# Performance work log

Measured on AMD Instinct MI355X. Metric: run time of the kernel, lower is better.

The kernel has to match this reference:

```python
import jax, jax.numpy as jnp
import numpy as np

C = 1.0
TEMPERATURE = 1.0
EPS = 1e-10
N, D = 8192, 512


def setup_inputs() -> dict:
    key = jax.random.key(0)
    k1, k2 = jax.random.split(key)
    # scale so embeddings lie inside the unit (Poincare) ball: norms ~0.5
    scale = 0.5 / np.sqrt(D)
    audio = jax.random.normal(k1, (N, D), dtype=jnp.float32) * scale
    text = jax.random.normal(k2, (N, D), dtype=jnp.float32) * scale
    labels = jnp.arange(N, dtype=jnp.int32)
    return {"audio_features": audio, "text_features": text, "labels": labels}


def _hyperbolic_similarity(a, b):
    # pairwise squared distance via norm expansion (avoids N x N x D tensor)
    a2 = jnp.sum(a * a, axis=-1)            # [N]
    b2 = jnp.sum(b * b, axis=-1)            # [M]
    diff_sq = a2[:, None] + b2[None, :] - 2.0 * (a @ b.T)  # [N, M]
    a2c = jnp.minimum(a2, 1.0 - EPS)
    b2c = jnp.minimum(b2, 1.0 - EPS)
    denom = jnp.maximum((1.0 - a2c)[:, None] * (1.0 - b2c)[None, :], EPS)
    arg = jnp.maximum(1.0 + 2.0 * diff_sq / denom, 1.0 + EPS)
    dist = jnp.arccosh(arg) / jnp.sqrt(jnp.asarray(C, a.dtype))
    return -dist / TEMPERATURE


def _cross_entropy(logits, labels):
    logp = jax.nn.log_softmax(logits, axis=-1)
    picked = jnp.take_along_axis(logp, labels[:, None], axis=-1)[:, 0]
    return -jnp.mean(picked)


def reference(audio_features, text_features, labels):
    sim = _hyperbolic_similarity(audio_features, text_features)  # [N, M]
    loss_audio = _cross_entropy(sim, labels)
    loss_text = _cross_entropy(sim.T, labels)
    return (loss_audio + loss_text) * 0.5
```

## Files before the change

kernel.cpp:

```cpp
#include <hip/hip_runtime.h>
#include <hip/hip_bf16.h>


#define NROWS 8192
#define DDIM  512
#define BM 128
#define BN 128
#define BK 64
#define NT (DDIM / BK)
#define LDSBUF 32768

typedef __attribute__((ext_vector_type(8))) short bf16x8;
typedef __attribute__((ext_vector_type(4))) float f32x4;

constexpr float EPSF = 1e-10f;

#define GLOAD_LDS16(g, l)                                                        \
    __builtin_amdgcn_global_load_lds(                                            \
        (const __attribute__((address_space(1))) void*)(g),                      \
        (__attribute__((address_space(3))) void*)(l), 16, 0, 0)

__device__ inline unsigned short f2bf(float f) {
    union { float f; unsigned int u; } x; x.f = f;
    unsigned int r = x.u + 0x7fffu + ((x.u >> 16) & 1u);
    return (unsigned short)(r >> 16);
}

__global__ __launch_bounds__(256) void convert_norms(const float* __restrict__ audio,
                                                     const float* __restrict__ text,
                                                     unsigned short* __restrict__ Ab,
                                                     unsigned short* __restrict__ Bb,
                                                     float* __restrict__ a2,
                                                     float* __restrict__ b2,
                                                     float* __restrict__ diag) {
    int wave = threadIdx.x >> 6;
    int lane = threadIdx.x & 63;
    int row  = blockIdx.x * 4 + wave;
    const float* ra = audio + (size_t)row * DDIM + lane * 8;
    const float* rt = text  + (size_t)row * DDIM + lane * 8;
    float4 a0 = *(const float4*)(ra), a1 = *(const float4*)(ra + 4);
    float4 t0 = *(const float4*)(rt), t1 = *(const float4*)(rt + 4);

    float sa = a0.x*a0.x + a0.y*a0.y + a0.z*a0.z + a0.w*a0.w
             + a1.x*a1.x + a1.y*a1.y + a1.z*a1.z + a1.w*a1.w;
    float st = t0.x*t0.x + t0.y*t0.y + t0.z*t0.z + t0.w*t0.w
             + t1.x*t1.x + t1.y*t1.y + t1.z*t1.z + t1.w*t1.w;
    float dt = a0.x*t0.x + a0.y*t0.y + a0.z*t0.z + a0.w*t0.w
             + a1.x*t1.x + a1.y*t1.y + a1.z*t1.z + a1.w*t1.w;

    unsigned short ua[8], ut[8];
    ua[0]=f2bf(a0.x); ua[1]=f2bf(a0.y); ua[2]=f2bf(a0.z); ua[3]=f2bf(a0.w);
    ua[4]=f2bf(a1.x); ua[5]=f2bf(a1.y); ua[6]=f2bf(a1.z); ua[7]=f2bf(a1.w);
    ut[0]=f2bf(t0.x); ut[1]=f2bf(t0.y); ut[2]=f2bf(t0.z); ut[3]=f2bf(t0.w);
    ut[4]=f2bf(t1.x); ut[5]=f2bf(t1.y); ut[6]=f2bf(t1.z); ut[7]=f2bf(t1.w);
    *(uint4*)(Ab + (size_t)row * DDIM + lane * 8) = *(const uint4*)ua;
    *(uint4*)(Bb + (size_t)row * DDIM + lane * 8) = *(const uint4*)ut;

    #pragma unroll
    for (int m = 1; m < 64; m <<= 1) {
        sa += __shfl_xor(sa, m);
        st += __shfl_xor(st, m);
        dt += __shfl_xor(dt, m);
    }
    if (lane == 0) {
        a2[row] = sa;
        b2[row] = st;
        float a2c  = fminf(sa, 1.0f - EPSF);
        float b2c  = fminf(st, 1.0f - EPSF);
        float diff = sa + st - 2.0f * dt;
        float den  = fmaxf((1.0f - a2c) * (1.0f - b2c), EPSF);
        float arg  = fmaxf(1.0f + 2.0f * diff / den, 1.0f + EPSF);
        diag[row]  = -logf(arg + sqrtf(arg * arg - 1.0f));
    }
}

__global__ __launch_bounds__(512, 4) void hyper_gemm(
    const unsigned short* __restrict__ A, const unsigned short* __restrict__ B,
    const float* __restrict__ a2, const float* __restrict__ b2,
    float* __restrict__ rowsum, float* __restrict__ colsum) {

    __shared__ char lds[2 * LDSBUF];

    const int tid  = threadIdx.x;
    const int lane = tid & 63;
    const int w    = tid >> 6;
    const int wm   = w >> 2;
    const int wn   = w & 3;

    const int bid = blockIdx.x;
    const int idx = bid >> 3;
    const int by  = (bid & 7) * 8 + (idx & 7);
    const int bx  = idx >> 3;
    const int i0 = by * BM;
    const int j0 = bx * BN;

    const int g  = lane >> 4;
    const int cl = lane & 15;

    const int srow = lane >> 3;
    const int scol = ((lane & 7) ^ srow) * 8;
    const char* aP[2]; const char* bP[2]; int ldsOff[2];
    #pragma unroll
    for (int c = 0; c < 2; ++c) {
        int row = w * 16 + c * 8 + srow;
        aP[c] = (const char*)(A + (size_t)(i0 + row) * DDIM + scol);
        bP[c] = (const char*)(B + (size_t)(j0 + row) * DDIM + scol);
        ldsOff[c] = w * 2048 + c * 1024;
    }

    int offA[4][2], offB[2][2];
    #pragma unroll
    for (int mi = 0; mi < 4; ++mi) {
        int rowA = wm * 64 + mi * 16 + cl;
        #pragma unroll
        for (int kh = 0; kh < 2; ++kh) {
            int cb = (kh * 32 + g * 8) * 2;
            offA[mi][kh] = rowA * 128 + (cb ^ ((rowA & 7) << 4));
        }
    }
    #pragma unroll
    for (int ni = 0; ni < 2; ++ni) {
        int rowB = wn * 32 + ni * 16 + cl;
        #pragma unroll
        for (int kh = 0; kh < 2; ++kh) {
            int cb = (kh * 32 + g * 8) * 2;
            offB[ni][kh] = 16384 + rowB * 128 + (cb ^ ((rowB & 7) << 4));
        }
    }

    f32x4 acc[4][2];
    #pragma unroll
    for (int mi = 0; mi < 4; ++mi)
        #pragma unroll
        for (int ni = 0; ni < 2; ++ni)
            acc[mi][ni] = (f32x4)0.0f;

#define STAGE(buf, t)                                                     \
    do {                                                                  \
        _Pragma("unroll")                                                 \
        for (int c = 0; c < 2; ++c) {                                     \
            GLOAD_LDS16(aP[c] + (t) * (BK * 2),                           \
                        lds + (buf) * LDSBUF + ldsOff[c]);                \
            GLOAD_LDS16(bP[c] + (t) * (BK * 2),                           \
                        lds + (buf) * LDSBUF + 16384 + ldsOff[c]);        \
        }                                                                 \
    } while (0)

#define COMPUTE(buf)                                                      \
    do {                                                                  \
        _Pragma("unroll")                                                 \
        for (int kh = 0; kh < 2; ++kh) {                                  \
            bf16x8 af[4], bv[2];                                          \
            _Pragma("unroll")                                             \
            for (int mi = 0; mi < 4; ++mi)                                \
                af[mi] = *(const bf16x8*)(lds + (buf) * LDSBUF + offA[mi][kh]); \
            _Pragma("unroll")                                             \
            for (int ni = 0; ni < 2; ++ni)                                \
                bv[ni] = *(const bf16x8*)(lds + (buf) * LDSBUF + offB[ni][kh]); \
            _Pragma("unroll")                                             \
            for (int mi = 0; mi < 4; ++mi)                                \
                _Pragma("unroll")                                         \
                for (int ni = 0; ni < 2; ++ni)                            \
                    acc[mi][ni] = __builtin_amdgcn_mfma_f32_16x16x32_bf16(\
                        af[mi], bv[ni], acc[mi][ni], 0, 0, 0);            \
        }                                                                 \
    } while (0)

    STAGE(0, 0);
    __syncthreads();
    #pragma unroll
    for (int t = 0; t < NT; ++t) {
        if (t + 1 < NT) STAGE((t + 1) & 1, t + 1);
        COMPUTE(t & 1);
        if (t + 1 < NT) __syncthreads();
    }
#undef STAGE
#undef COMPUTE

    float B2c[2], fb[2];
    #pragma unroll
    for (int ni = 0; ni < 2; ++ni) {
        float B2 = b2[j0 + wn * 32 + ni * 16 + cl];
        B2c[ni] = B2;
        fb[ni] = __builtin_amdgcn_rcpf(1.0f - fminf(B2, 1.0f - EPSF));
    }

    float cp[2] = {0.f, 0.f};
    #pragma unroll
    for (int mi = 0; mi < 4; ++mi) {
        #pragma unroll
        for (int reg = 0; reg < 4; ++reg) {
            int   gi  = i0 + wm * 64 + mi * 16 + g * 4 + reg;
            float A2  = a2[gi];
            float fa  = 2.0f * __builtin_amdgcn_rcpf(1.0f - fminf(A2, 1.0f - EPSF));
            float rsum = 0.f;
            #pragma unroll
            for (int ni = 0; ni < 2; ++ni) {
                float dot  = acc[mi][ni][reg];
                float diff = fmaf(-2.0f, dot, A2 + B2c[ni]);
                float arg  = fmaf(diff * fa, fb[ni], 1.0f);
                arg = fmaxf(arg, 1.0f);
                float sq = sqrtf(fmaf(arg, arg, -1.0f));
                float e  = arg - sq;
                rsum += e;
                cp[ni] += e;
            }
            float v = rsum;
            v += __shfl_xor(v, 1); v += __shfl_xor(v, 2);
            v += __shfl_xor(v, 4); v += __shfl_xor(v, 8);
            if (cl == 0) atomicAdd(&rowsum[gi], v);
        }
    }
    #pragma unroll
    for (int ni = 0; ni < 2; ++ni) {
        float v = cp[ni];
        v += __shfl_xor(v, 16); v += __shfl_xor(v, 32);
        if (g == 0) atomicAdd(&colsum[j0 + wn * 32 + ni * 16 + cl], v);
    }
}

__global__ __launch_bounds__(1024) void finalize(const float* __restrict__ rowsum,
                                                 const float* __restrict__ colsum,
                                                 const float* __restrict__ diag,
                                                 float* __restrict__ out) {
    float s = 0.f;
    for (int i = threadIdx.x; i < NROWS; i += 1024)
        s += logf(rowsum[i]) + logf(colsum[i]) - 2.0f * diag[i];
    __shared__ float red[16];
    int lane = threadIdx.x & 63, wv = threadIdx.x >> 6;
    #pragma unroll
    for (int m = 1; m < 64; m <<= 1) s += __shfl_xor(s, m);
    if (lane == 0) red[wv] = s;
    __syncthreads();
    if (threadIdx.x == 0) {
        float t = 0.f;
        #pragma unroll
        for (int k = 0; k < 16; ++k) t += red[k];
        out[0] = t / (2.0f * NROWS);
    }
}

extern "C" void kernel_launch(void* const* d_in, const int* in_sizes, int n_in,
                              void* d_out, int out_size, void* d_ws, size_t ws_size,
                              hipStream_t stream) {
    const float* audio = (const float*)d_in[0];
    const float* text  = (const float*)d_in[1];
    float* out = (float*)d_out;

    char* ws = (char*)d_ws;
    const size_t BF = (size_t)NROWS * DDIM * sizeof(unsigned short);
    unsigned short* Abf = (unsigned short*)ws;
    unsigned short* Bbf = (unsigned short*)(ws + BF);
    float* a2     = (float*)(ws + 2 * BF);
    float* b2     = a2 + NROWS;
    float* rowsum = b2 + NROWS;
    float* colsum = rowsum + NROWS;
    float* diag   = colsum + NROWS;

    hipMemsetAsync(rowsum, 0, 2 * NROWS * sizeof(float), stream);
    convert_norms<<<NROWS / 4, 256, 0, stream>>>(audio, text, Abf, Bbf, a2, b2, diag);
    hyper_gemm<<<(NROWS / BM) * (NROWS / BN), 512, 0, stream>>>(Abf, Bbf, a2, b2, rowsum, colsum);
    finalize<<<1, 1024, 0, stream>>>(rowsum, colsum, diag, out);
}
```

Measured before the change: 229.1 us.

## Switch GEMM operands from bf16 to scaled fp8 e4m3 MFMA and fold memset

New measurement: 212.6 us. 1.08x faster.

```diff
diff --git a/kernel.cpp b/kernel.cpp
--- a/kernel.cpp
+++ b/kernel.cpp
@@ -6,33 +6,48 @@
 #define DDIM  512
 #define BM 128
 #define BN 128
-#define BK 64
+#define BK 128
 #define NT (DDIM / BK)
 #define LDSBUF 32768
 
-typedef __attribute__((ext_vector_type(8))) short bf16x8;
 typedef __attribute__((ext_vector_type(4))) float f32x4;
 
 constexpr float EPSF = 1e-10f;
+constexpr float DOT_SCALE = 1.0f / 1024.0f;
 
 #define GLOAD_LDS16(g, l)                                                        \
     __builtin_amdgcn_global_load_lds(                                            \
         (const __attribute__((address_space(1))) void*)(g),                      \
         (__attribute__((address_space(3))) void*)(l), 16, 0, 0)
 
-__device__ inline unsigned short f2bf(float f) {
+__device__ inline unsigned int f2e4m3(float f) {
     union { float f; unsigned int u; } x; x.f = f;
-    unsigned int r = x.u + 0x7fffu + ((x.u >> 16) & 1u);
-    return (unsigned short)(r >> 16);
+    unsigned int s = (x.u >> 24) & 0x80u;
+    float af = __builtin_fabsf(f);
+    unsigned int r;
+    if (af >= 0.015625f) {
+        unsigned int m = x.u & 0x7fffffffu;
+        m += 0x000fffffu + ((m >> 20) & 1u);
+        r = ((m >> 20) - (120u << 3)) & 0x7fu;
+    } else {
+        int q = (int)rintf(af * 512.0f);
+        r = (unsigned int)q;
+    }
+    return r | s;
 }
 
 __global__ __launch_bounds__(256) void convert_norms(const float* __restrict__ audio,
                                                      const float* __restrict__ text,
-                                                     unsigned short* __restrict__ Ab,
-                                                     unsigned short* __restrict__ Bb,
+                                                     unsigned char* __restrict__ Aq,
+                                                     unsigned char* __restrict__ Bq,
                                                      float* __restrict__ a2,
                                                      float* __restrict__ b2,
-                                                     float* __restrict__ diag) {
+                                                     float* __restrict__ diag,
+                                                     float* __restrict__ zbuf) {
+    if (blockIdx.x < 32) {
+        int z = blockIdx.x * 512 + threadIdx.x * 2;
+        *(float2*)(zbuf + z) = make_float2(0.f, 0.f);
+    }
     int wave = threadIdx.x >> 6;
     int lane = threadIdx.x & 63;
     int row  = blockIdx.x * 4 + wave;
@@ -48,13 +63,17 @@
     float dt = a0.x*t0.x + a0.y*t0.y + a0.z*t0.z + a0.w*t0.w
              + a1.x*t1.x + a1.y*t1.y + a1.z*t1.z + a1.w*t1.w;
 
-    unsigned short ua[8], ut[8];
-    ua[0]=f2bf(a0.x); ua[1]=f2bf(a0.y); ua[2]=f2bf(a0.z); ua[3]=f2bf(a0.w);
-    ua[4]=f2bf(a1.x); ua[5]=f2bf(a1.y); ua[6]=f2bf(a1.z); ua[7]=f2bf(a1.w);
-    ut[0]=f2bf(t0.x); ut[1]=f2bf(t0.y); ut[2]=f2bf(t0.z); ut[3]=f2bf(t0.w);
-    ut[4]=f2bf(t1.x); ut[5]=f2bf(t1.y); ut[6]=f2bf(t1.z); ut[7]=f2bf(t1.w);
-    *(uint4*)(Ab + (size_t)row * DDIM + lane * 8) = *(const uint4*)ua;
-    *(uint4*)(Bb + (size_t)row * DDIM + lane * 8) = *(const uint4*)ut;
+    uint2 pa, pt;
+    pa.x = f2e4m3(a0.x*32.f) | (f2e4m3(a0.y*32.f) << 8) |
+           (f2e4m3(a0.z*32.f) << 16) | (f2e4m3(a0.w*32.f) << 24);
+    pa.y = f2e4m3(a1.x*32.f) | (f2e4m3(a1.y*32.f) << 8) |
+           (f2e4m3(a1.z*32.f) << 16) | (f2e4m3(a1.w*32.f) << 24);
+    pt.x = f2e4m3(t0.x*32.f) | (f2e4m3(t0.y*32.f) << 8) |
+           (f2e4m3(t0.z*32.f) << 16) | (f2e4m3(t0.w*32.f) << 24);
+    pt.y = f2e4m3(t1.x*32.f) | (f2e4m3(t1.y*32.f) << 8) |
+           (f2e4m3(t1.z*32.f) << 16) | (f2e4m3(t1.w*32.f) << 24);
+    *(uint2*)(Aq + (size_t)row * DDIM + lane * 8) = pa;
+    *(uint2*)(Bq + (size_t)row * DDIM + lane * 8) = pt;
 
     #pragma unroll
     for (int m = 1; m < 64; m <<= 1) {
@@ -75,7 +94,7 @@
 }
 
 __global__ __launch_bounds__(512, 4) void hyper_gemm(
-    const unsigned short* __restrict__ A, const unsigned short* __restrict__ B,
+    const unsigned char* __restrict__ A, const unsigned char* __restrict__ B,
     const float* __restrict__ a2, const float* __restrict__ b2,
     float* __restrict__ rowsum, float* __restrict__ colsum) {
 
@@ -98,34 +117,32 @@
     const int cl = lane & 15;
 
     const int srow = lane >> 3;
-    const int scol = ((lane & 7) ^ srow) * 8;
-    const char* aP[2]; const char* bP[2]; int ldsOff[2];
+    const int scol = (((lane & 7) ^ srow)) * 16;
+    const unsigned char* aP[2]; const unsigned char* bP[2]; int ldsOff[2];
     #pragma unroll
     for (int c = 0; c < 2; ++c) {
         int row = w * 16 + c * 8 + srow;
-        aP[c] = (const char*)(A + (size_t)(i0 + row) * DDIM + scol);
-        bP[c] = (const char*)(B + (size_t)(j0 + row) * DDIM + scol);
+        aP[c] = A + (size_t)(i0 + row) * DDIM + scol;
+        bP[c] = B + (size_t)(j0 + row) * DDIM + scol;
         ldsOff[c] = w * 2048 + c * 1024;
     }
 
-    int offA[4][2], offB[2][2];
+    int addrA[4][4], addrB[2][4];
     #pragma unroll
     for (int mi = 0; mi < 4; ++mi) {
-        int rowA = wm * 64 + mi * 16 + cl;
-        #pragma unroll
-        for (int kh = 0; kh < 2; ++kh) {
-            int cb = (kh * 32 + g * 8) * 2;
-            offA[mi][kh] = rowA * 128 + (cb ^ ((rowA & 7) << 4));
-        }
+        int row = wm * 64 + mi * 16 + cl;
+        int s = (row & 7) << 4;
+        #pragma unroll
+        for (int ks = 0; ks < 4; ++ks)
+            addrA[mi][ks] = row * 128 + ((ks * 32 + g * 8) ^ s);
     }
     #pragma unroll
     for (int ni = 0; ni < 2; ++ni) {
-        int rowB = wn * 32 + ni * 16 + cl;
-        #pragma unroll
-        for (int kh = 0; kh < 2; ++kh) {
-            int cb = (kh * 32 + g * 8) * 2;
-            offB[ni][kh] = 16384 + rowB * 128 + (cb ^ ((rowB & 7) << 4));
-        }
+        int row = wn * 32 + ni * 16 + cl;
+        int s = (row & 7) << 4;
+        #pragma unroll
+        for (int ks = 0; ks < 4; ++ks)
+            addrB[ni][ks] = 16384 + row * 128 + ((ks * 32 + g * 8) ^ s);
     }
 
     f32x4 acc[4][2];
@@ -139,9 +156,9 @@
     do {                                                                  \
         _Pragma("unroll")                                                 \
         for (int c = 0; c < 2; ++c) {                                     \
-            GLOAD_LDS16(aP[c] + (t) * (BK * 2),                           \
+            GLOAD_LDS16(aP[c] + (t) * BK,                                 \
                         lds + (buf) * LDSBUF + ldsOff[c]);                \
-            GLOAD_LDS16(bP[c] + (t) * (BK * 2),                           \
+            GLOAD_LDS16(bP[c] + (t) * BK,                                 \
                         lds + (buf) * LDSBUF + 16384 + ldsOff[c]);        \
         }                                                                 \
     } while (0)
@@ -149,20 +166,20 @@
 #define COMPUTE(buf)                                                      \
     do {                                                                  \
         _Pragma("unroll")                                                 \
-        for (int kh = 0; kh < 2; ++kh) {                                  \
-            bf16x8 af[4], bv[2];                                          \
+        for (int ks = 0; ks < 4; ++ks) {                                  \
+            long av[4]; long bv[2];                                       \
             _Pragma("unroll")                                             \
             for (int mi = 0; mi < 4; ++mi)                                \
-                af[mi] = *(const bf16x8*)(lds + (buf) * LDSBUF + offA[mi][kh]); \
+                av[mi] = *(const long*)(lds + (buf) * LDSBUF + addrA[mi][ks]); \
             _Pragma("unroll")                                             \
             for (int ni = 0; ni < 2; ++ni)                                \
-                bv[ni] = *(const bf16x8*)(lds + (buf) * LDSBUF + offB[ni][kh]); \
+                bv[ni] = *(const long*)(lds + (buf) * LDSBUF + addrB[ni][ks]); \
             _Pragma("unroll")                                             \
             for (int mi = 0; mi < 4; ++mi)                                \
                 _Pragma("unroll")                                         \
                 for (int ni = 0; ni < 2; ++ni)                            \
-                    acc[mi][ni] = __builtin_amdgcn_mfma_f32_16x16x32_bf16(\
-                        af[mi], bv[ni], acc[mi][ni], 0, 0, 0);            \
+                    acc[mi][ni] = __builtin_amdgcn_mfma_f32_16x16x32_fp8_fp8( \
+                        av[mi], bv[ni], acc[mi][ni], 0, 0, 0);            \
         }                                                                 \
     } while (0)
 
@@ -197,7 +214,7 @@
             #pragma unroll
             for (int ni = 0; ni < 2; ++ni) {
                 float dot  = acc[mi][ni][reg];
-                float diff = fmaf(-2.0f, dot, A2 + B2c[ni]);
+                float diff = fmaf(-2.0f * DOT_SCALE, dot, A2 + B2c[ni]);
                 float arg  = fmaf(diff * fa, fb[ni], 1.0f);
                 arg = fmaxf(arg, 1.0f);
                 float sq = sqrtf(fmaf(arg, arg, -1.0f));
@@ -248,17 +265,16 @@
     float* out = (float*)d_out;
 
     char* ws = (char*)d_ws;
-    const size_t BF = (size_t)NROWS * DDIM * sizeof(unsigned short);
-    unsigned short* Abf = (unsigned short*)ws;
-    unsigned short* Bbf = (unsigned short*)(ws + BF);
+    const size_t BF = (size_t)NROWS * DDIM;
+    unsigned char* Aq = (unsigned char*)ws;
+    unsigned char* Bq = (unsigned char*)(ws + BF);
     float* a2     = (float*)(ws + 2 * BF);
     float* b2     = a2 + NROWS;
     float* rowsum = b2 + NROWS;
     float* colsum = rowsum + NROWS;
     float* diag   = colsum + NROWS;
 
-    hipMemsetAsync(rowsum, 0, 2 * NROWS * sizeof(float), stream);
-    convert_norms<<<NROWS / 4, 256, 0, stream>>>(audio, text, Abf, Bbf, a2, b2, diag);
-    hyper_gemm<<<(NROWS / BM) * (NROWS / BN), 512, 0, stream>>>(Abf, Bbf, a2, b2, rowsum, colsum);
+    convert_norms<<<NROWS / 4, 256, 0, stream>>>(audio, text, Aq, Bq, a2, b2, diag, rowsum);
+    hyper_gemm<<<(NROWS / BM) * (NROWS / BN), 512, 0, stream>>>(Aq, Bq, a2, b2, rowsum, colsum);
     finalize<<<1, 1024, 0, stream>>>(rowsum, colsum, diag, out);
 }
```
